# Kernel optimization log

Hardware: AMD Instinct MI355X
Metric: run time of the kernel (lower is better)

## Reference

```python
import jax, jax.numpy as jnp
import numpy as np

N_EMBD = 1024
N_HEAD = 16
HORIZON = 64
HS = N_EMBD // N_HEAD        # 64
BD = max(HS // 4, 16)        # 16


def setup_inputs() -> dict:
    key = jax.random.key(0)
    ks = jax.random.split(key, 12)
    s = 0.02
    B, T = 2, 1024
    return {
        "x": jax.random.normal(ks[0], (B, T, N_EMBD), jnp.float32),
        "W_disp": jax.random.normal(ks[1], (N_EMBD, N_HEAD * BD), jnp.float32) * s,
        "W_val": jax.random.normal(ks[2], (N_EMBD, N_EMBD), jnp.float32) * s,
        "rel_pos_emb": jax.random.normal(ks[3], (HORIZON, BD), jnp.float32) * s,
        "W_strain": jax.random.normal(ks[4], (BD, BD), jnp.float32) * s,
        "W_pos": jax.random.normal(ks[5], (BD, BD), jnp.float32) * s,
        "W_bond": jax.random.normal(ks[6], (BD, 1), jnp.float32) * s,
        "W_dmg": jax.random.normal(ks[7], (BD, BD), jnp.float32) * s,
        "b_dmg": jnp.zeros((BD,), jnp.float32),
        "W_dmg_out": jax.random.normal(ks[8], (BD, 1), jnp.float32) * s,
        "b_dmg_out": jnp.full((1,), -3.0, jnp.float32),  # nn.init.constant_(damage_out.bias, -3.0)
        "W_cproj": jax.random.normal(ks[9], (N_EMBD, N_EMBD), jnp.float32) * s,
    }


def _windows(t, delta):
    # t: (B, nh, T, D) -> (B, nh, T, delta, D); causal sliding window via left pad
    B, nh, T, D = t.shape
    padded = jnp.pad(t, ((0, 0), (0, 0), (delta - 1, 0), (0, 0)))
    idx = jnp.arange(T)[:, None] + jnp.arange(delta)[None, :]  # (T, delta)
    return padded[:, :, idx]  # gather over time axis


def reference(x, W_disp, W_val, rel_pos_emb, W_strain, W_pos, W_bond,
              W_dmg, b_dmg, W_dmg_out, b_dmg_out, W_cproj):
    B, T, C = x.shape
    nh, bd, hs = N_HEAD, BD, HS
    delta = min(HORIZON, T)

    disp = (x @ W_disp).reshape(B, T, nh, bd).transpose(0, 2, 1, 3)  # (B,nh,T,bd)
    val = (x @ W_val).reshape(B, T, nh, hs).transpose(0, 2, 1, 3)    # (B,nh,T,hs)

    disp_win = _windows(disp, delta)  # (B,nh,T,delta,bd)
    val_win = _windows(val, delta)    # (B,nh,T,delta,hs)

    # causal mask: window slot w for token t maps to position t - delta + 1 + w
    cmask = (jnp.arange(T)[:, None] - delta + 1 + jnp.arange(delta)[None, :]) >= 0  # (T,delta)

    strain = disp_win - disp[:, :, :, None, :]  # (B,nh,T,delta,bd)
    rel_emb = rel_pos_emb[:delta]               # (delta,bd)

    bond_act = jax.nn.gelu(strain @ W_strain + rel_emb @ W_pos, approximate=False)
    bond_logits = (bond_act @ W_bond)[..., 0]   # (B,nh,T,delta)

    damage_act = jax.nn.gelu(strain @ W_dmg + b_dmg, approximate=False)
    damage = jax.nn.sigmoid((damage_act @ W_dmg_out)[..., 0] + b_dmg_out[0])

    logits = bond_logits - 10.0 * damage
    logits = jnp.where(cmask[None, None], logits, -jnp.inf)
    weights = jax.nn.softmax(logits, axis=-1)

    out = jnp.einsum('bntd,bntde->bnte', weights, val_win)  # (B,nh,T,hs)
    out = out.transpose(0, 2, 1, 3).reshape(B, T, C)
    return out @ W_cproj
```

## Files before the change

### kernel.cpp

```cpp
#include <hip/hip_runtime.h>
#include <hip/hip_bf16.h>
#include <hip/hip_fp16.h>
#include <math.h>

#define TB   2
#define TT   1024
#define TC   1024
#define NH   16
#define HS   64
#define BDI  16
#define DLT  64
#define GK   1024
#define NDV  1536
#define PQS  1152

typedef __attribute__((ext_vector_type(8))) short short8;
typedef __attribute__((ext_vector_type(4))) float floatx4;
typedef __hip_bfloat16 bf16;

__device__ __forceinline__ unsigned bfbits(float x) {
    bf16 h = __float2bfloat16(x);
    return (unsigned)*(unsigned short*)&h;
}
__device__ __forceinline__ unsigned short hfbits(float x) {
    __half h = __float2half_rn(x);
    return *(unsigned short*)&h;
}
__device__ __forceinline__ unsigned packh2(float lo, float hi) {
    __half2 h = __floats2half2_rn(lo, hi);
    return *(unsigned*)&h;
}

__device__ __forceinline__ __half2 gelu_pk(__half2 x, __half2 kc1, __half2 kc2,
                                           __half2 khalf) {
    __half2 y = __hmul2(x, x);
    __half2 p = __hfma2(y, kc2, kc1);
    return __hfma2(x, khalf, __hmul2(y, p));
}

__device__ __forceinline__ void gload_lds16(const void* g, void* l) {
    __builtin_amdgcn_global_load_lds(
        (const __attribute__((address_space(1))) unsigned int*)(unsigned long long)g,
        (__attribute__((address_space(3))) unsigned int*)(unsigned int)(unsigned long long)l,
        16, 0, 0);
}

__device__ __forceinline__ void tpose_body(const float* __restrict__ in,
                                           bf16* __restrict__ outp,
                                           int k0, int n0, int N,
                                           float (*tile)[33], int tid) {
    const int tx = tid & 31, ty4 = (tid >> 5) * 4;
#pragma unroll
    for (int i = 0; i < 4; i++)
        tile[ty4 + i][tx] = in[(long long)(k0 + ty4 + i) * N + n0 + tx];
    __syncthreads();
#pragma unroll
    for (int i = 0; i < 4; i++)
        outp[(long long)(n0 + ty4 + i) * TC + k0 + tx] = __float2bfloat16(tile[tx][ty4 + i]);
}

__global__ __launch_bounds__(256) void prep_k(
    const float* __restrict__ x, const float* __restrict__ Wdisp,
    const float* __restrict__ Wval, const float* __restrict__ Wc,
    const float* __restrict__ rel, const float* __restrict__ Wp,
    const float* __restrict__ Ws, const float* __restrict__ Wd,
    bf16* __restrict__ xb, bf16* __restrict__ Wdvt, bf16* __restrict__ Wct,
    float* __restrict__ peG) {
    __shared__ float tile[32][33];
    const int blk = blockIdx.x, tid = threadIdx.x;
    if (blk < 2048) {
        int i = blk * 1024 + tid * 4;
        float4 v = *(const float4*)(x + i);
        ushort4 u;
        u.x = (unsigned short)bfbits(v.x); u.y = (unsigned short)bfbits(v.y);
        u.z = (unsigned short)bfbits(v.z); u.w = (unsigned short)bfbits(v.w);
        *(ushort4*)(xb + i) = u;
    } else if (blk < 4096) {
        int idx = (blk - 2048) * 256 + tid;
        int k = idx & 1023, n = idx >> 10;
        int h = n >> 5, pq = (n >> 4) & 1, d2 = n & 15;
        const float* Wsel = pq ? Wd : Ws;
        const float* wrow = Wdisp + (size_t)k * 256 + h * 16;
        float s = 0.f;
#pragma unroll
        for (int d = 0; d < BDI; d++)
            s = fmaf(wrow[d], Wsel[d * BDI + d2], s);
        Wdvt[(size_t)n * TC + k] = __float2bfloat16(s);
    } else if (blk < 5120) {
        int l = blk - 4096;
        tpose_body(Wval, Wdvt + (size_t)512 * TC, (l >> 5) * 32, (l & 31) * 32, TC, tile, tid);
    } else if (blk < 6144) {
        int l = blk - 5120;
        tpose_body(Wc, Wct, (l >> 5) * 32, (l & 31) * 32, TC, tile, tid);
    } else {
        int idx = (blk - 6144) * 256 + tid;
        int j = idx >> 4, d = idx & 15;
        float s = 0.f;
#pragma unroll
        for (int k = 0; k < BDI; k++)
            s += rel[j * BDI + k] * Wp[k * BDI + d];
        peG[idx] = s;
    }
}

template <int ID>
__global__ __launch_bounds__(256) void mfma_gemm_k(const bf16* __restrict__ A,
                                                   const bf16* __restrict__ Bt,
                                                   float* __restrict__ C,
                                                   bf16* __restrict__ valT,
                                                   unsigned* __restrict__ pqT,
                                                   int M, int N, int nbx) {
    __shared__ __align__(16) bf16 As[2][64 * 128];
    __shared__ __align__(16) bf16 Bs[2][64 * 128];
    const int tid = threadIdx.x;
    const int w = tid >> 6, lane = tid & 63;

    const int xcd = blockIdx.x & 7, s0 = blockIdx.x >> 3;
    const int l = xcd * (gridDim.x >> 3) + s0;
    const int row0 = (l / nbx) * 64, col0 = (l % nbx) * 64;
    const int wm = (w >> 1) * 32, wn = (w & 1) * 32;

    const bf16* gA[4];
    const bf16* gB[4];
    int lofs[4];
#pragma unroll
    for (int p = 0; p < 4; p++) {
        int u = (p * 4 + w) * 64 + lane;
        int r = u >> 4, s = u & 15;
        int c = s ^ (r & 15);
        gA[p] = A  + (long long)(row0 + r) * GK + c * 8;
        gB[p] = Bt + (long long)(col0 + r) * GK + c * 8;
        lofs[p] = (p * 4 + w) * 512;
    }

    floatx4 acc[2][2] = {};
    const int rA = lane & 15, quad = lane >> 4;

#pragma unroll
    for (int p = 0; p < 4; p++) {
        gload_lds16(gA[p], &As[0][lofs[p]]);
        gload_lds16(gB[p], &Bs[0][lofs[p]]);
    }

    int cur = 0;
    for (int k0 = 0; k0 < GK; k0 += 128) {
        __syncthreads();
        if (k0 + 128 < GK) {
#pragma unroll
            for (int p = 0; p < 4; p++) {
                gload_lds16(gA[p] + k0 + 128, &As[cur ^ 1][lofs[p]]);
                gload_lds16(gB[p] + k0 + 128, &Bs[cur ^ 1][lofs[p]]);
            }
        }
        const bf16* Ac = As[cur];
        const bf16* Bc = Bs[cur];
#pragma unroll
        for (int kh = 0; kh < 4; kh++) {
            const int g = kh * 4 + quad;
            short8 af[2], bfr[2];
#pragma unroll
            for (int i = 0; i < 2; i++) {
                af[i]  = *(const short8*)&Ac[(wm + i * 16 + rA) * 128 + ((g ^ rA) * 8)];
                bfr[i] = *(const short8*)&Bc[(wn + i * 16 + rA) * 128 + ((g ^ rA) * 8)];
            }
#pragma unroll
            for (int i = 0; i < 2; i++)
#pragma unroll
                for (int j = 0; j < 2; j++)
                    acc[i][j] = __builtin_amdgcn_mfma_f32_16x16x32_bf16(af[i], bfr[j], acc[i][j], 0, 0, 0);
        }
        cur ^= 1;
    }
    const int cn = lane & 15, rq = (lane >> 4) * 4;
    if (ID == 1 && col0 < 512) {
        __syncthreads();
        unsigned short (*eT)[68] = (unsigned short (*)[68])As;
#pragma unroll
        for (int i = 0; i < 2; i++)
#pragma unroll
            for (int j = 0; j < 2; j++) {
                int e = wn + j * 16 + cn;
                int t = wm + i * 16 + rq;
#pragma unroll
                for (int r = 0; r < 4; r++)
                    eT[e][t + r] = hfbits(acc[i][j][r]);
            }
        __syncthreads();
        const int hbase = col0 >> 5;
        const int bb = row0 >> 10, t0g = row0 & (TT - 1);
        for (int idx = tid; idx < 512; idx += 256) {
            int r = idx >> 4, c4 = idx & 15;
            int hl = r >> 4, d2 = r & 15, tt = c4 * 4;
            const unsigned short* pr = &eT[hl * 32 + d2][tt];
            const unsigned short* qr = &eT[hl * 32 + 16 + d2][tt];
            uint4 o;
            o.x = (unsigned)pr[0] | ((unsigned)qr[0] << 16);
            o.y = (unsigned)pr[1] | ((unsigned)qr[1] << 16);
            o.z = (unsigned)pr[2] | ((unsigned)qr[2] << 16);
            o.w = (unsigned)pr[3] | ((unsigned)qr[3] << 16);
            unsigned* dst = pqT + (size_t)((bb * NH + hbase + hl) * BDI + d2) * PQS
                          + 64 + t0g + tt;
            *(uint4*)dst = o;
        }
    } else if (ID == 1) {
        __syncthreads();
        unsigned short (*eT)[68] = (unsigned short (*)[68])As;
#pragma unroll
        for (int i = 0; i < 2; i++)
#pragma unroll
            for (int j = 0; j < 2; j++) {
                int e = wn + j * 16 + cn;
                int t = wm + i * 16 + rq;
                uint2 st;
                st.x = bfbits(acc[i][j][0]) | (bfbits(acc[i][j][1]) << 16);
                st.y = bfbits(acc[i][j][2]) | (bfbits(acc[i][j][3]) << 16);
                *(uint2*)&eT[e][t] = st;
            }
        __syncthreads();
        const int hh = (col0 - 512) >> 6;
        const int bb = row0 >> 10;
        const int trow0 = row0 & (TT - 1);
        bf16* base = valT + (size_t)((bb * NH + hh) * HS) * TT + trow0;
        for (int idx = tid; idx < 512; idx += 256) {
            int e = idx >> 3, c = idx & 7;
            *(uint4*)(base + (size_t)e * TT + c * 8) = *(const uint4*)&eT[e][c * 8];
        }
    } else {
#pragma unroll
        for (int i = 0; i < 2; i++)
#pragma unroll
            for (int j = 0; j < 2; j++) {
                long long base = (long long)(row0 + wm + i * 16 + rq) * N + col0 + wn + j * 16 + cn;
#pragma unroll
                for (int r = 0; r < 4; r++)
                    C[base + (long long)r * N] = acc[i][j][r];
            }
    }
}

__global__ __launch_bounds__(256) void attn_k(
    const unsigned* __restrict__ pqT,
    const bf16* __restrict__ valT,
    const float* __restrict__ peG,
    const float* __restrict__ b_dmg,
    const float* __restrict__ W_bond,
    const float* __restrict__ W_dmg_out,
    const float* __restrict__ b_dmg_out,
    bf16* __restrict__ attnout) {
    __shared__ __align__(16) unsigned       sPQ[16][80];
    __shared__ __align__(16) unsigned       sPEB[64][17];
    __shared__ __align__(16) unsigned short sWgtS[16][104];

    const int tid = threadIdx.x;
    const int wave = tid >> 6, lane = tid & 63;
    const int xcd = blockIdx.x & 7, slot = blockIdx.x >> 3;
    const int bh = xcd * 4 + (slot >> 6);
    const int t0 = (slot & 63) * 16;
    const int h = bh & (NH - 1);
    const int b = bh >> 4;

    {
        const unsigned* gbase = pqT + (size_t)(b * NH + h) * BDI * PQS + t0;
        for (int task = tid; task < 320; task += 256) {
            int d2 = task / 20, c = task - d2 * 20;
            gload_lds16(gbase + (size_t)d2 * PQS + 4 * c,
                        (char*)sPQ + (task & ~63) * 16);
        }
    }
    if (tid < 208) ((int4*)sWgtS)[tid] = make_int4(0, 0, 0, 0);
    {
        int j = tid >> 2, q4 = (tid & 3) * 4;
        float4 pv = *(const float4*)(peG + j * BDI + q4);
        float4 bv = *(const float4*)(b_dmg + q4);
        sPEB[j][q4 + 0] = packh2(pv.x, bv.x);
        sPEB[j][q4 + 1] = packh2(pv.y, bv.y);
        sPEB[j][q4 + 2] = packh2(pv.z, bv.z);
        sPEB[j][q4 + 3] = packh2(pv.w, bv.w);
    }
    __half2 w2[16];
#pragma unroll
    for (int q = 0; q < 4; q++) {
        float4 wb = *(const float4*)(W_bond + 4 * q);
        float4 wd = *(const float4*)(W_dmg_out + 4 * q);
        w2[4 * q + 0] = __floats2half2_rn(wb.x, wd.x);
        w2[4 * q + 1] = __floats2half2_rn(wb.y, wd.y);
        w2[4 * q + 2] = __floats2half2_rn(wb.z, wd.z);
        w2[4 * q + 3] = __floats2half2_rn(wb.w, wd.w);
    }
    const float bdo0 = b_dmg_out[0];
    const __half2 kc1   = __floats2half2_rn(0.3989422804f, 0.3989422804f);
    const __half2 kc2   = __floats2half2_rn(-0.06649038006f, -0.06649038006f);
    const __half2 khalf = __floats2half2_rn(0.5f, 0.5f);

    __syncthreads();

    __half2 pb[16];
#pragma unroll
    for (int d2 = 0; d2 < 16; d2++) pb[d2] = *(const __half2*)&sPEB[lane][d2];

#pragma unroll
    for (int s = 0; s < 4; s++) {
        const int tl = 4 * wave + s;
        __half2 acc = __floats2half2_rn(0.f, 0.f);
#pragma unroll
        for (int d2 = 0; d2 < 16; d2++) {
            unsigned wv = sPQ[d2][tl + 1 + lane];
            unsigned cv = sPQ[d2][tl + 64];
            __half2 x = __hsub2(*(const __half2*)&wv, *(const __half2*)&cv);
            x = __hadd2(x, pb[d2]);
            acc = __hfma2(gelu_pk(x, kc1, kc2, khalf), w2[d2], acc);
        }
        float bond = __low2float(acc), dmgv = __high2float(acc);
        float damage = 1.f / (1.f + __expf(-(dmgv + bdo0)));
        const bool valid = (t0 + tl - 63 + lane) >= 0;
        float e = valid ? __expf(bond - 10.f * damage) : 0.f;
        float sm = e;
#pragma unroll
        for (int off = 32; off >= 1; off >>= 1) sm += __shfl_xor(sm, off);
        sWgtS[tl][tl + 1 + lane] = (unsigned short)bfbits(e / sm);
    }
    __syncthreads();

    const int m = lane & 15, quad = lane >> 4;
    const floatx4 zf = {0.f, 0.f, 0.f, 0.f};
    const bf16* vbase = valT + ((size_t)(b * NH + h) * HS + 16 * wave + m) * TT;
    floatx4 acc = zf;
#pragma unroll
    for (int c = 0; c < 3; c++) {
        int toff = t0 - 64 + c * 32 + quad * 8;
        toff = toff < 0 ? 0 : (toff > TT - 8 ? TT - 8 : toff);
        short8 afr = *(const short8*)&sWgtS[m][c * 32 + quad * 8];
        short8 bfr = *(const short8*)(vbase + toff);
        acc = __builtin_amdgcn_mfma_f32_16x16x32_bf16(afr, bfr, acc, 0, 0, 0);
    }
    const int e0 = 16 * wave + m;
#pragma unroll
    for (int r = 0; r < 4; r++) {
        int tau = quad * 4 + r;
        attnout[(long long)(b * TT + t0 + tau) * TC + h * HS + e0] = __float2bfloat16(acc[r]);
    }
}

extern "C" void kernel_launch(void* const* d_in, const int* in_sizes, int n_in,
                              void* d_out, int out_size, void* d_ws, size_t ws_size,
                              hipStream_t stream) {
    const float* x      = (const float*)d_in[0];
    const float* W_disp = (const float*)d_in[1];
    const float* W_val  = (const float*)d_in[2];
    const float* rel    = (const float*)d_in[3];
    const float* Ws     = (const float*)d_in[4];
    const float* Wp     = (const float*)d_in[5];
    const float* Wb     = (const float*)d_in[6];
    const float* Wd     = (const float*)d_in[7];
    const float* bd_    = (const float*)d_in[8];
    const float* Wdo    = (const float*)d_in[9];
    const float* bdo    = (const float*)d_in[10];
    const float* Wc     = (const float*)d_in[11];
    float* out = (float*)d_out;

    const int M = TB * TT;
    char* ws = (char*)d_ws;
    bf16*     xb    = (bf16*)ws;
    bf16*     attnb = (bf16*)ws;
    bf16*     Wdvt  = (bf16*)(ws + (size_t)4 * 1024 * 1024);
    bf16*     Wct   = (bf16*)(ws + (size_t)7 * 1024 * 1024);
    bf16*     valT  = (bf16*)(ws + (size_t)9 * 1024 * 1024);
    unsigned* pqT   = (unsigned*)(ws + (size_t)13 * 1024 * 1024);
    float*    peG   = (float*)(ws + (size_t)15872 * 1024);

    dim3 blk(256);
    prep_k<<<6148, blk, 0, stream>>>(x, W_disp, W_val, Wc, rel, Wp, Ws, Wd,
                                     xb, Wdvt, Wct, peG);
    mfma_gemm_k<1><<<(M / 64) * (NDV / 64), blk, 0, stream>>>(xb, Wdvt, nullptr,
                                                              valT, pqT, M, 0, NDV / 64);
    attn_k<<<(TB * NH * TT) / 16, blk, 0, stream>>>(pqT, valT, peG, bd_, Wb,
                                                    Wdo, bdo, attnb);
    mfma_gemm_k<2><<<(M / 64) * (TC / 64), blk, 0, stream>>>(attnb, Wct, out,
                                                             nullptr, nullptr, M, TC, TC / 64);
}
```

Measured before the change: 127.2 us.

## Restructure fused disp-weight prep and halve GEMM K-tile for occupancy

The prep kernel's fused W_disp·W_strain/W_dmg product is reworked so each of 32 blocks handles one head and one projection. The small 16x16 weight is staged in shared memory and each thread computes four K rows with vectorized loads and packed bf16 stores, where before 2048 blocks each did scalar strided loads. Separately, the MFMA GEMM K-tile drops from 128 to 64 with a matching XOR swizzle, which halves LDS use. A launch-bounds occupancy hint of 4 is added to allow more resident blocks, at the cost of twice as many loop iterations and barriers.

```diff
diff --git a/kernel.cpp b/kernel.cpp
--- a/kernel.cpp
+++ b/kernel.cpp
@@ -75,25 +75,45 @@
         u.x = (unsigned short)bfbits(v.x); u.y = (unsigned short)bfbits(v.y);
         u.z = (unsigned short)bfbits(v.z); u.w = (unsigned short)bfbits(v.w);
         *(ushort4*)(xb + i) = u;
-    } else if (blk < 4096) {
-        int idx = (blk - 2048) * 256 + tid;
-        int k = idx & 1023, n = idx >> 10;
-        int h = n >> 5, pq = (n >> 4) & 1, d2 = n & 15;
+    } else if (blk < 2080) {
+        int l = blk - 2048, hh = l >> 1, pq = l & 1;
         const float* Wsel = pq ? Wd : Ws;
-        const float* wrow = Wdisp + (size_t)k * 256 + h * 16;
-        float s = 0.f;
-#pragma unroll
-        for (int d = 0; d < BDI; d++)
-            s = fmaf(wrow[d], Wsel[d * BDI + d2], s);
-        Wdvt[(size_t)n * TC + k] = __float2bfloat16(s);
-    } else if (blk < 5120) {
-        int l = blk - 4096;
+        float (*wsl)[17] = (float (*)[17])tile;
+        wsl[tid >> 4][tid & 15] = Wsel[tid];
+        __syncthreads();
+        const float* wbase = Wdisp + (size_t)(tid * 4) * 256 + hh * 16;
+        float s[16][4];
+#pragma unroll
+        for (int kk = 0; kk < 4; kk++) {
+            float wrow[16];
+            *(float4*)&wrow[0]  = *(const float4*)(wbase + kk * 256);
+            *(float4*)&wrow[4]  = *(const float4*)(wbase + kk * 256 + 4);
+            *(float4*)&wrow[8]  = *(const float4*)(wbase + kk * 256 + 8);
+            *(float4*)&wrow[12] = *(const float4*)(wbase + kk * 256 + 12);
+#pragma unroll
+            for (int d2 = 0; d2 < 16; d2++) {
+                float acc = 0.f;
+#pragma unroll
+                for (int d = 0; d < 16; d++) acc = fmaf(wrow[d], wsl[d][d2], acc);
+                s[d2][kk] = acc;
+            }
+        }
+        bf16* outb = Wdvt + (size_t)(hh * 32 + pq * 16) * TC + tid * 4;
+#pragma unroll
+        for (int d2 = 0; d2 < 16; d2++) {
+            ushort4 u;
+            u.x = (unsigned short)bfbits(s[d2][0]); u.y = (unsigned short)bfbits(s[d2][1]);
+            u.z = (unsigned short)bfbits(s[d2][2]); u.w = (unsigned short)bfbits(s[d2][3]);
+            *(ushort4*)(outb + (size_t)d2 * TC) = u;
+        }
+    } else if (blk < 3104) {
+        int l = blk - 2080;
         tpose_body(Wval, Wdvt + (size_t)512 * TC, (l >> 5) * 32, (l & 31) * 32, TC, tile, tid);
-    } else if (blk < 6144) {
-        int l = blk - 5120;
+    } else if (blk < 4128) {
+        int l = blk - 3104;
         tpose_body(Wc, Wct, (l >> 5) * 32, (l & 31) * 32, TC, tile, tid);
     } else {
-        int idx = (blk - 6144) * 256 + tid;
+        int idx = (blk - 4128) * 256 + tid;
         int j = idx >> 4, d = idx & 15;
         float s = 0.f;
 #pragma unroll
@@ -104,14 +124,14 @@
 }
 
 template <int ID>
-__global__ __launch_bounds__(256) void mfma_gemm_k(const bf16* __restrict__ A,
-                                                   const bf16* __restrict__ Bt,
-                                                   float* __restrict__ C,
-                                                   bf16* __restrict__ valT,
-                                                   unsigned* __restrict__ pqT,
-                                                   int M, int N, int nbx) {
-    __shared__ __align__(16) bf16 As[2][64 * 128];
-    __shared__ __align__(16) bf16 Bs[2][64 * 128];
+__global__ __launch_bounds__(256, 4) void mfma_gemm_k(const bf16* __restrict__ A,
+                                                      const bf16* __restrict__ Bt,
+                                                      float* __restrict__ C,
+                                                      bf16* __restrict__ valT,
+                                                      unsigned* __restrict__ pqT,
+                                                      int M, int N, int nbx) {
+    __shared__ __align__(16) bf16 As[2][64 * 64];
+    __shared__ __align__(16) bf16 Bs[2][64 * 64];
     const int tid = threadIdx.x;
     const int w = tid >> 6, lane = tid & 63;
 
@@ -120,14 +140,14 @@
     const int row0 = (l / nbx) * 64, col0 = (l % nbx) * 64;
     const int wm = (w >> 1) * 32, wn = (w & 1) * 32;
 
-    const bf16* gA[4];
-    const bf16* gB[4];
-    int lofs[4];
-#pragma unroll
-    for (int p = 0; p < 4; p++) {
+    const bf16* gA[2];
+    const bf16* gB[2];
+    int lofs[2];
+#pragma unroll
+    for (int p = 0; p < 2; p++) {
         int u = (p * 4 + w) * 64 + lane;
-        int r = u >> 4, s = u & 15;
-        int c = s ^ (r & 15);
+        int r = u >> 3, s = u & 7;
+        int c = s ^ (r & 7);
         gA[p] = A  + (long long)(row0 + r) * GK + c * 8;
         gB[p] = Bt + (long long)(col0 + r) * GK + c * 8;
         lofs[p] = (p * 4 + w) * 512;
@@ -137,31 +157,31 @@
     const int rA = lane & 15, quad = lane >> 4;
 
 #pragma unroll
-    for (int p = 0; p < 4; p++) {
+    for (int p = 0; p < 2; p++) {
         gload_lds16(gA[p], &As[0][lofs[p]]);
         gload_lds16(gB[p], &Bs[0][lofs[p]]);
     }
 
     int cur = 0;
-    for (int k0 = 0; k0 < GK; k0 += 128) {
-        __syncthreads();
-        if (k0 + 128 < GK) {
-#pragma unroll
-            for (int p = 0; p < 4; p++) {
-                gload_lds16(gA[p] + k0 + 128, &As[cur ^ 1][lofs[p]]);
-                gload_lds16(gB[p] + k0 + 128, &Bs[cur ^ 1][lofs[p]]);
+    for (int k0 = 0; k0 < GK; k0 += 64) {
+        __syncthreads();
+        if (k0 + 64 < GK) {
+#pragma unroll
+            for (int p = 0; p < 2; p++) {
+                gload_lds16(gA[p] + k0 + 64, &As[cur ^ 1][lofs[p]]);
+                gload_lds16(gB[p] + k0 + 64, &Bs[cur ^ 1][lofs[p]]);
             }
         }
         const bf16* Ac = As[cur];
         const bf16* Bc = Bs[cur];
 #pragma unroll
-        for (int kh = 0; kh < 4; kh++) {
+        for (int kh = 0; kh < 2; kh++) {
             const int g = kh * 4 + quad;
             short8 af[2], bfr[2];
 #pragma unroll
             for (int i = 0; i < 2; i++) {
-                af[i]  = *(const short8*)&Ac[(wm + i * 16 + rA) * 128 + ((g ^ rA) * 8)];
-                bfr[i] = *(const short8*)&Bc[(wn + i * 16 + rA) * 128 + ((g ^ rA) * 8)];
+                af[i]  = *(const short8*)&Ac[(wm + i * 16 + rA) * 64 + ((g ^ (rA & 7)) * 8)];
+                bfr[i] = *(const short8*)&Bc[(wn + i * 16 + rA) * 64 + ((g ^ (rA & 7)) * 8)];
             }
 #pragma unroll
             for (int i = 0; i < 2; i++)
@@ -369,7 +389,7 @@
     float*    peG   = (float*)(ws + (size_t)15872 * 1024);
 
     dim3 blk(256);
-    prep_k<<<6148, blk, 0, stream>>>(x, W_disp, W_val, Wc, rel, Wp, Ws, Wd,
+    prep_k<<<4132, blk, 0, stream>>>(x, W_disp, W_val, Wc, rel, Wp, Ws, Wd,
                                      xb, Wdvt, Wct, peG);
     mfma_gemm_k<1><<<(M / 64) * (NDV / 64), blk, 0, stream>>>(xb, Wdvt, nullptr,
                                                               valT, pqT, M, 0, NDV / 64);
```

Measured after the change: 127.6 us. Within noise of the previous version (+0.4%).
